# Kernel tuning notes

Hardware: AMD Instinct MI355X
Metric: run time of the kernel (lower is better)

Reference implementation:

```python
import math
import jax, jax.numpy as jnp
import numpy as np

N = 131072   # flattened batch (agents * timesteps)
D = 4        # input_dim
F = 64       # num_freq_bands
H = 128      # hidden_dim
EPS = 1e-5


def _layer_norm(x, g, b):
    mu = jnp.mean(x, axis=-1, keepdims=True)
    var = jnp.var(x, axis=-1, keepdims=True)
    return (x - mu) * jax.lax.rsqrt(var + EPS) * g + b


def setup_inputs() -> dict:
    key = jax.random.key(0)
    ks = jax.random.split(key, 8)
    fin = 2 * F + 1  # 129
    return {
        "continuous_inputs": jax.random.normal(ks[0], (N, D), dtype=jnp.float32),
        "freqs": jax.random.normal(ks[1], (D, F), dtype=jnp.float32),
        # per-dim MLP ensemble, stacked over D
        "w1": jax.random.normal(ks[2], (D, fin, H), dtype=jnp.float32) * (1.0 / math.sqrt(fin)),
        "b1": jnp.zeros((D, H), dtype=jnp.float32),
        "ln1_g": jnp.ones((D, H), dtype=jnp.float32),
        "ln1_b": jnp.zeros((D, H), dtype=jnp.float32),
        "w2": jax.random.normal(ks[3], (D, H, H), dtype=jnp.float32) * (1.0 / math.sqrt(H)),
        "b2": jnp.zeros((D, H), dtype=jnp.float32),
        # to_out head
        "out_ln_g": jnp.ones((H,), dtype=jnp.float32),
        "out_ln_b": jnp.zeros((H,), dtype=jnp.float32),
        "w3": jax.random.normal(ks[4], (H, H), dtype=jnp.float32) * (1.0 / math.sqrt(H)),
        "b3": jnp.zeros((H,), dtype=jnp.float32),
    }


def reference(continuous_inputs, freqs, w1, b1, ln1_g, ln1_b, w2, b2,
              out_ln_g, out_ln_b, w3, b3):
    # x: [N, D, F] = input[..., None] * freqs * 2*pi
    x = continuous_inputs[..., None] * freqs * (2.0 * math.pi)
    # Fourier features: [N, D, 2F+1]
    feat = jnp.concatenate([jnp.cos(x), jnp.sin(x), continuous_inputs[..., None]], axis=-1)
    # batched per-dim MLP: Linear -> LayerNorm -> ReLU -> Linear, then sum over D
    h = jnp.einsum("ndf,dfh->ndh", feat, w1) + b1          # [N, D, H]
    h = _layer_norm(h, ln1_g, ln1_b)
    h = jax.nn.relu(h)
    h = jnp.einsum("ndh,dhk->ndk", h, w2) + b2             # [N, D, H]
    emb = jnp.sum(h, axis=1)                               # [N, H]
    # to_out: LayerNorm -> ReLU -> Linear
    out = _layer_norm(emb, out_ln_g, out_ln_b)
    out = jax.nn.relu(out)
    return out @ w3 + b3
```

## Files before the change

kernel.cpp:

```cpp
#include <hip/hip_runtime.h>
#include <hip/hip_bf16.h>
#include <math.h>

typedef __bf16 bf16t;
typedef __bf16 bf8v __attribute__((ext_vector_type(8)));
typedef float  f4v  __attribute__((ext_vector_type(4)));
typedef unsigned int u32;
typedef u32 u4v __attribute__((ext_vector_type(4)));

#define DD  4
#define FF  64
#define HH  128
#define FIN 129
#define MT  64

#define AS1 __attribute__((address_space(1)))
#define AS3 __attribute__((address_space(3)))

#define P_FREQS 0
#define P_B1    256
#define P_W1L   768
#define P_OG    1280
#define P_OB    1408
#define P_B3    1536
#define P_TOT   1664

__device__ __forceinline__ int swz(int row, int k) {
  return row * HH + ((((k >> 3) ^ (row & 7)) << 3) | (k & 7));
}

__global__ void prep_weights(const float* __restrict__ w1,
                             const float* __restrict__ w2,
                             const float* __restrict__ w3,
                             bf16t* __restrict__ w1t,
                             bf16t* __restrict__ w2t,
                             bf16t* __restrict__ w3t,
                             float* __restrict__ w1last) {
  int i = blockIdx.x * blockDim.x + threadIdx.x;
  if (i < DD * HH * HH) {
    int d = i >> 14, n = (i >> 7) & 127, k = i & 127;
    w1t[i] = (bf16t)w1[(d * FIN + k) * HH + n];
    w2t[i] = (bf16t)w2[(d * HH + k) * HH + n];
  }
  if (i < HH * HH) {
    int n = i >> 7, k = i & 127;
    w3t[i] = (bf16t)w3[k * HH + n];
  }
  if (i < DD * HH) {
    int d = i >> 7, n = i & 127;
    w1last[i] = w1[(d * FIN + 128) * HH + n];
  }
}

__device__ __forceinline__ void stage_w_async(const bf16t* __restrict__ w,
                                              bf16t* __restrict__ ldsW,
                                              int tid, int wave) {
  int g0 = (tid & ~15) | ((tid & 15) ^ ((tid >> 4) & 7));
  const bf16t* src = w + g0 * 8;
  bf16t* dst = ldsW + wave * 64 * 8;
  #pragma unroll
  for (int j = 0; j < 8; ++j) {
    __builtin_amdgcn_global_load_lds((const AS1 void*)(src + j * 2048),
                                     (AS3 void*)(dst + j * 2048), 16, 0, 0);
  }
}

__device__ __forceinline__ u32 pack2(float a, float b) {
  union { bf16t h; unsigned short u; } ua, ub;
  ua.h = (bf16t)a; ub.h = (bf16t)b;
  return ((u32)ub.u << 16) | (u32)ua.u;
}

__device__ __forceinline__ void xpose_pack(const f4v (&h)[8], bf8v (&bb)[4],
                                           int l15, int q) {
  const int lA = l15 + 16 * ((2 * q) & 3);
  const int lB = l15 + 16 * ((2 * q + 1) & 3);
  const bool hiq = (q >= 2);
  #pragma unroll
  for (int K = 0; K < 4; ++K) {
    u32 pa0 = pack2(h[2 * K][0],     h[2 * K][1]);
    u32 pa1 = pack2(h[2 * K][2],     h[2 * K][3]);
    u32 pb0 = pack2(h[2 * K + 1][0], h[2 * K + 1][1]);
    u32 pb1 = pack2(h[2 * K + 1][2], h[2 * K + 1][3]);
    u32 w0a = __shfl(pa0, lA), w0b = __shfl(pb0, lA);
    u32 w1a = __shfl(pa1, lA), w1b = __shfl(pb1, lA);
    u32 w2a = __shfl(pa0, lB), w2b = __shfl(pb0, lB);
    u32 w3a = __shfl(pa1, lB), w3b = __shfl(pb1, lB);
    u4v wv;
    wv.x = hiq ? w0b : w0a;
    wv.y = hiq ? w1b : w1a;
    wv.z = hiq ? w2b : w2a;
    wv.w = hiq ? w3b : w3a;
    union { u4v w; bf8v v; } cv;
    cv.w = wv;
    bb[K] = cv.v;
  }
}

__launch_bounds__(256, 4)
__global__ void fourier_mlp(
    const float* __restrict__ cont,
    const float* __restrict__ freqs,
    const float* __restrict__ b1,
    const float* __restrict__ ln1g,
    const float* __restrict__ ln1b,
    const float* __restrict__ b2,
    const float* __restrict__ outg,
    const float* __restrict__ outb,
    const float* __restrict__ b3,
    const bf16t* __restrict__ w1t,
    const bf16t* __restrict__ w2t,
    const bf16t* __restrict__ w3t,
    const float* __restrict__ w1last,
    float* __restrict__ out)
{
  __shared__ __align__(16) bf16t ldsW[HH * HH];
  __shared__ __align__(16) float ldsP[P_TOT];

  const int tid  = threadIdx.x;
  const int lane = tid & 63;
  const int wave = tid >> 6;
  const int q    = lane >> 4;
  const int l15  = lane & 15;
  const int rowbase = blockIdx.x * MT;
  const int wrow = wave * 16;

  stage_w_async(w1t, ldsW, tid, wave);
  ldsP[P_FREQS + tid] = freqs[tid];
  #pragma unroll
  for (int i = 0; i < 2; ++i) {
    int j = tid + i * 256;
    ldsP[P_B1 + j]  = b1[j];
    ldsP[P_W1L + j] = w1last[j];
  }
  if (tid < 128) {
    ldsP[P_OG + tid] = outg[tid];
    ldsP[P_OB + tid] = outb[tid];
    ldsP[P_B3 + tid] = b3[tid];
  }
  f4v call = *(const f4v*)&cont[(rowbase + wrow + l15) * DD];

  const f4v fzero = {0.0f, 0.0f, 0.0f, 0.0f};
  f4v emb[8];
  #pragma unroll
  for (int nt = 0; nt < 8; ++nt) emb[nt] = fzero;

  __syncthreads();

  for (int d = 0; d < DD; ++d) {
    bf8v fB[4];
    {
      const float c = call[d];
      #pragma unroll
      for (int hf = 0; hf < 2; ++hf) {
        f4v f0 = *(const f4v*)&ldsP[P_FREQS + d * FF + hf * 32 + q * 8];
        f4v f1 = *(const f4v*)&ldsP[P_FREQS + d * FF + hf * 32 + q * 8 + 4];
        #pragma unroll
        for (int u = 0; u < 8; ++u) {
          float fv = (u < 4) ? f0[u] : f1[u - 4];
          float a = c * fv;
          float t = a - floorf(a);
          fB[hf][u]     = (bf16t)__builtin_amdgcn_cosf(t);
          fB[2 + hf][u] = (bf16t)__builtin_amdgcn_sinf(t);
        }
      }
    }
    __syncthreads();

    f4v acc[8];
    #pragma unroll
    for (int nt = 0; nt < 8; ++nt) acc[nt] = fzero;
    #pragma unroll
    for (int K = 0; K < 4; ++K)
      #pragma unroll
      for (int nt = 0; nt < 8; ++nt) {
        bf8v wf = *(const bf8v*)&ldsW[swz(nt * 16 + l15, K * 32 + q * 8)];
        acc[nt] = __builtin_amdgcn_mfma_f32_16x16x32_bf16(wf, fB[K], acc[nt], 0, 0, 0);
      }
    __syncthreads();
    stage_w_async(w2t + d * HH * HH, ldsW, tid, wave);

    bf8v bB[4];
    {
      const float c = call[d];
      float s = 0.0f, ss = 0.0f;
      #pragma unroll
      for (int nt = 0; nt < 8; ++nt) {
        f4v b1v = *(const f4v*)&ldsP[P_B1 + d * HH + nt * 16 + q * 4];
        f4v w1l = *(const f4v*)&ldsP[P_W1L + d * HH + nt * 16 + q * 4];
        #pragma unroll
        for (int r = 0; r < 4; ++r) {
          float v = acc[nt][r] + b1v[r] + c * w1l[r];
          acc[nt][r] = v;
          s += v; ss += v * v;
        }
      }
      s  += __shfl_xor(s, 16);  s  += __shfl_xor(s, 32);
      ss += __shfl_xor(ss, 16); ss += __shfl_xor(ss, 32);
      float mu   = s * (1.0f / 128.0f);
      float var  = ss * (1.0f / 128.0f) - mu * mu;
      float rstd = rsqrtf(var + 1e-5f);
      #pragma unroll
      for (int nt = 0; nt < 8; ++nt) {
        f4v gv = *(const f4v*)&ln1g[d * HH + nt * 16 + q * 4];
        f4v bv = *(const f4v*)&ln1b[d * HH + nt * 16 + q * 4];
        #pragma unroll
        for (int r = 0; r < 4; ++r) {
          float v = (acc[nt][r] - mu) * rstd * gv[r] + bv[r];
          acc[nt][r] = fmaxf(v, 0.0f);
        }
      }
      xpose_pack(acc, bB, l15, q);
    }
    __syncthreads();

    #pragma unroll
    for (int K = 0; K < 4; ++K)
      #pragma unroll
      for (int nt = 0; nt < 8; ++nt) {
        bf8v wf = *(const bf8v*)&ldsW[swz(nt * 16 + l15, K * 32 + q * 8)];
        emb[nt] = __builtin_amdgcn_mfma_f32_16x16x32_bf16(wf, bB[K], emb[nt], 0, 0, 0);
      }
    #pragma unroll
    for (int nt = 0; nt < 8; ++nt) {
      f4v b2v = *(const f4v*)&b2[d * HH + nt * 16 + q * 4];
      emb[nt] += b2v;
    }
    __syncthreads();
    stage_w_async(d < 3 ? (w1t + (d + 1) * HH * HH) : w3t, ldsW, tid, wave);
  }

  bf8v bB[4];
  {
    float s = 0.0f, ss = 0.0f;
    #pragma unroll
    for (int nt = 0; nt < 8; ++nt)
      #pragma unroll
      for (int r = 0; r < 4; ++r) {
        float v = emb[nt][r];
        s += v; ss += v * v;
      }
    s  += __shfl_xor(s, 16);  s  += __shfl_xor(s, 32);
    ss += __shfl_xor(ss, 16); ss += __shfl_xor(ss, 32);
    float mu   = s * (1.0f / 128.0f);
    float var  = ss * (1.0f / 128.0f) - mu * mu;
    float rstd = rsqrtf(var + 1e-5f);
    #pragma unroll
    for (int nt = 0; nt < 8; ++nt) {
      f4v gv = *(const f4v*)&ldsP[P_OG + nt * 16 + q * 4];
      f4v bv = *(const f4v*)&ldsP[P_OB + nt * 16 + q * 4];
      #pragma unroll
      for (int r = 0; r < 4; ++r) {
        float v = (emb[nt][r] - mu) * rstd * gv[r] + bv[r];
        emb[nt][r] = fmaxf(v, 0.0f);
      }
    }
    xpose_pack(emb, bB, l15, q);
  }
  __syncthreads();

  f4v acc[8];
  #pragma unroll
  for (int nt = 0; nt < 8; ++nt) acc[nt] = fzero;
  #pragma unroll
  for (int K = 0; K < 4; ++K)
    #pragma unroll
    for (int nt = 0; nt < 8; ++nt) {
      bf8v wf = *(const bf8v*)&ldsW[swz(nt * 16 + l15, K * 32 + q * 8)];
      acc[nt] = __builtin_amdgcn_mfma_f32_16x16x32_bf16(wf, bB[K], acc[nt], 0, 0, 0);
    }

  #pragma unroll
  for (int nt = 0; nt < 8; ++nt) {
    f4v b3v = *(const f4v*)&ldsP[P_B3 + nt * 16 + q * 4];
    f4v o = acc[nt] + b3v;
    *(f4v*)&out[(rowbase + wrow + l15) * HH + nt * 16 + q * 4] = o;
  }
}

extern "C" void kernel_launch(void* const* d_in, const int* in_sizes, int n_in,
                              void* d_out, int out_size, void* d_ws, size_t ws_size,
                              hipStream_t stream) {
  const float* cont  = (const float*)d_in[0];
  const float* freqs = (const float*)d_in[1];
  const float* w1    = (const float*)d_in[2];
  const float* b1    = (const float*)d_in[3];
  const float* ln1g  = (const float*)d_in[4];
  const float* ln1b  = (const float*)d_in[5];
  const float* w2    = (const float*)d_in[6];
  const float* b2    = (const float*)d_in[7];
  const float* outg  = (const float*)d_in[8];
  const float* outb  = (const float*)d_in[9];
  const float* w3    = (const float*)d_in[10];
  const float* b3    = (const float*)d_in[11];
  float* out = (float*)d_out;

  bf16t* w1t = (bf16t*)d_ws;
  bf16t* w2t = w1t + DD * HH * HH;
  bf16t* w3t = w2t + DD * HH * HH;
  float* w1last = (float*)((char*)d_ws + (2 * DD * HH * HH + HH * HH) * sizeof(bf16t));

  prep_weights<<<(DD * HH * HH + 255) / 256, 256, 0, stream>>>(
      w1, w2, w3, w1t, w2t, w3t, w1last);

  int n_rows = in_sizes[0] / DD;
  int grid = n_rows / MT;
  fourier_mlp<<<grid, 256, 0, stream>>>(
      cont, freqs, b1, ln1g, ln1b, b2, outg, outb, b3,
      w1t, w2t, w3t, w1last, out);
}
```

Before: 179.2 us.

## Read weights directly from global memory instead of staging through LDS

Removes the LDS staging of the weight matrices and small parameter vectors, along with all block-wide barriers. Each wave now loads its MFMA weight fragments straight from global memory and relies on L1/L2 caching, since every block reads the same weights. Launch bounds are relaxed from 4 to 2 blocks per SM, which allows more registers per thread. The cost is more global and cache traffic per MFMA operand and less latency hiding at lower occupancy, in exchange for no synchronisation stalls and no LDS footprint.

New measurement: 410.8 us. +129.2%, slower.

```diff
diff --git a/kernel.cpp b/kernel.cpp
--- a/kernel.cpp
+++ b/kernel.cpp
@@ -13,21 +13,6 @@
 #define HH  128
 #define FIN 129
 #define MT  64
-
-#define AS1 __attribute__((address_space(1)))
-#define AS3 __attribute__((address_space(3)))
-
-#define P_FREQS 0
-#define P_B1    256
-#define P_W1L   768
-#define P_OG    1280
-#define P_OB    1408
-#define P_B3    1536
-#define P_TOT   1664
-
-__device__ __forceinline__ int swz(int row, int k) {
-  return row * HH + ((((k >> 3) ^ (row & 7)) << 3) | (k & 7));
-}
 
 __global__ void prep_weights(const float* __restrict__ w1,
                              const float* __restrict__ w2,
@@ -49,19 +34,6 @@
   if (i < DD * HH) {
     int d = i >> 7, n = i & 127;
     w1last[i] = w1[(d * FIN + 128) * HH + n];
-  }
-}
-
-__device__ __forceinline__ void stage_w_async(const bf16t* __restrict__ w,
-                                              bf16t* __restrict__ ldsW,
-                                              int tid, int wave) {
-  int g0 = (tid & ~15) | ((tid & 15) ^ ((tid >> 4) & 7));
-  const bf16t* src = w + g0 * 8;
-  bf16t* dst = ldsW + wave * 64 * 8;
-  #pragma unroll
-  for (int j = 0; j < 8; ++j) {
-    __builtin_amdgcn_global_load_lds((const AS1 void*)(src + j * 2048),
-                                     (AS3 void*)(dst + j * 2048), 16, 0, 0);
   }
 }
 
@@ -97,7 +69,7 @@
   }
 }
 
-__launch_bounds__(256, 4)
+__launch_bounds__(256, 2)
 __global__ void fourier_mlp(
     const float* __restrict__ cont,
     const float* __restrict__ freqs,
@@ -114,38 +86,19 @@
     const float* __restrict__ w1last,
     float* __restrict__ out)
 {
-  __shared__ __align__(16) bf16t ldsW[HH * HH];
-  __shared__ __align__(16) float ldsP[P_TOT];
-
   const int tid  = threadIdx.x;
   const int lane = tid & 63;
   const int wave = tid >> 6;
   const int q    = lane >> 4;
   const int l15  = lane & 15;
-  const int rowbase = blockIdx.x * MT;
-  const int wrow = wave * 16;
-
-  stage_w_async(w1t, ldsW, tid, wave);
-  ldsP[P_FREQS + tid] = freqs[tid];
-  #pragma unroll
-  for (int i = 0; i < 2; ++i) {
-    int j = tid + i * 256;
-    ldsP[P_B1 + j]  = b1[j];
-    ldsP[P_W1L + j] = w1last[j];
-  }
-  if (tid < 128) {
-    ldsP[P_OG + tid] = outg[tid];
-    ldsP[P_OB + tid] = outb[tid];
-    ldsP[P_B3 + tid] = b3[tid];
-  }
-  f4v call = *(const f4v*)&cont[(rowbase + wrow + l15) * DD];
+  const int row0 = blockIdx.x * MT + wave * 16;
+
+  const f4v call = *(const f4v*)&cont[(row0 + l15) * DD];
 
   const f4v fzero = {0.0f, 0.0f, 0.0f, 0.0f};
   f4v emb[8];
   #pragma unroll
   for (int nt = 0; nt < 8; ++nt) emb[nt] = fzero;
-
-  __syncthreads();
 
   for (int d = 0; d < DD; ++d) {
     bf8v fB[4];
@@ -153,8 +106,8 @@
       const float c = call[d];
       #pragma unroll
       for (int hf = 0; hf < 2; ++hf) {
-        f4v f0 = *(const f4v*)&ldsP[P_FREQS + d * FF + hf * 32 + q * 8];
-        f4v f1 = *(const f4v*)&ldsP[P_FREQS + d * FF + hf * 32 + q * 8 + 4];
+        f4v f0 = *(const f4v*)&freqs[d * FF + hf * 32 + q * 8];
+        f4v f1 = *(const f4v*)&freqs[d * FF + hf * 32 + q * 8 + 4];
         #pragma unroll
         for (int u = 0; u < 8; ++u) {
           float fv = (u < 4) ? f0[u] : f1[u - 4];
@@ -165,8 +118,8 @@
         }
       }
     }
-    __syncthreads();
-
+
+    const bf16t* w1d = w1t + d * HH * HH;
     f4v acc[8];
     #pragma unroll
     for (int nt = 0; nt < 8; ++nt) acc[nt] = fzero;
@@ -174,11 +127,9 @@
     for (int K = 0; K < 4; ++K)
       #pragma unroll
       for (int nt = 0; nt < 8; ++nt) {
-        bf8v wf = *(const bf8v*)&ldsW[swz(nt * 16 + l15, K * 32 + q * 8)];
+        bf8v wf = *(const bf8v*)&w1d[(nt * 16 + l15) * HH + K * 32 + q * 8];
         acc[nt] = __builtin_amdgcn_mfma_f32_16x16x32_bf16(wf, fB[K], acc[nt], 0, 0, 0);
       }
-    __syncthreads();
-    stage_w_async(w2t + d * HH * HH, ldsW, tid, wave);
 
     bf8v bB[4];
     {
@@ -186,8 +137,8 @@
       float s = 0.0f, ss = 0.0f;
       #pragma unroll
       for (int nt = 0; nt < 8; ++nt) {
-        f4v b1v = *(const f4v*)&ldsP[P_B1 + d * HH + nt * 16 + q * 4];
-        f4v w1l = *(const f4v*)&ldsP[P_W1L + d * HH + nt * 16 + q * 4];
+        f4v b1v = *(const f4v*)&b1[d * HH + nt * 16 + q * 4];
+        f4v w1l = *(const f4v*)&w1last[d * HH + nt * 16 + q * 4];
         #pragma unroll
         for (int r = 0; r < 4; ++r) {
           float v = acc[nt][r] + b1v[r] + c * w1l[r];
@@ -212,13 +163,13 @@
       }
       xpose_pack(acc, bB, l15, q);
     }
-    __syncthreads();
-
+
+    const bf16t* w2d = w2t + d * HH * HH;
     #pragma unroll
     for (int K = 0; K < 4; ++K)
       #pragma unroll
       for (int nt = 0; nt < 8; ++nt) {
-        bf8v wf = *(const bf8v*)&ldsW[swz(nt * 16 + l15, K * 32 + q * 8)];
+        bf8v wf = *(const bf8v*)&w2d[(nt * 16 + l15) * HH + K * 32 + q * 8];
         emb[nt] = __builtin_amdgcn_mfma_f32_16x16x32_bf16(wf, bB[K], emb[nt], 0, 0, 0);
       }
     #pragma unroll
@@ -226,8 +177,6 @@
       f4v b2v = *(const f4v*)&b2[d * HH + nt * 16 + q * 4];
       emb[nt] += b2v;
     }
-    __syncthreads();
-    stage_w_async(d < 3 ? (w1t + (d + 1) * HH * HH) : w3t, ldsW, tid, wave);
   }
 
   bf8v bB[4];
@@ -247,8 +196,8 @@
     float rstd = rsqrtf(var + 1e-5f);
     #pragma unroll
     for (int nt = 0; nt < 8; ++nt) {
-      f4v gv = *(const f4v*)&ldsP[P_OG + nt * 16 + q * 4];
-      f4v bv = *(const f4v*)&ldsP[P_OB + nt * 16 + q * 4];
+      f4v gv = *(const f4v*)&outg[nt * 16 + q * 4];
+      f4v bv = *(const f4v*)&outb[nt * 16 + q * 4];
       #pragma unroll
       for (int r = 0; r < 4; ++r) {
         float v = (emb[nt][r] - mu) * rstd * gv[r] + bv[r];
@@ -257,7 +206,6 @@
     }
     xpose_pack(emb, bB, l15, q);
   }
-  __syncthreads();
 
   f4v acc[8];
   #pragma unroll
@@ -266,15 +214,15 @@
   for (int K = 0; K < 4; ++K)
     #pragma unroll
     for (int nt = 0; nt < 8; ++nt) {
-      bf8v wf = *(const bf8v*)&ldsW[swz(nt * 16 + l15, K * 32 + q * 8)];
+      bf8v wf = *(const bf8v*)&w3t[(nt * 16 + l15) * HH + K * 32 + q * 8];
       acc[nt] = __builtin_amdgcn_mfma_f32_16x16x32_bf16(wf, bB[K], acc[nt], 0, 0, 0);
     }
 
   #pragma unroll
   for (int nt = 0; nt < 8; ++nt) {
-    f4v b3v = *(const f4v*)&ldsP[P_B3 + nt * 16 + q * 4];
+    f4v b3v = *(const f4v*)&b3[nt * 16 + q * 4];
     f4v o = acc[nt] + b3v;
-    *(f4v*)&out[(rowbase + wrow + l15) * HH + nt * 16 + q * 4] = o;
+    *(f4v*)&out[(row0 + l15) * HH + nt * 16 + q * 4] = o;
   }
 }
 
```
